# Kernel optimization log

Hardware: AMD Instinct MI355X
Metric: run time of the kernel (lower is better)

Reference implementation:

```python
import jax, jax.numpy as jnp
import numpy as np

NUM_GRIDS = 8
GRID = jnp.linspace(-2.0, 2.0, NUM_GRIDS)
DENOM = 4.0 / (NUM_GRIDS - 1)
H, D = 8, 64
Q_DIM = K_DIM = V_DIM = 512
TOT = H * D


def fastkan(x, ln_s, ln_b, sw, bw, bb):
    # LayerNorm over last dim
    mu = jnp.mean(x, axis=-1, keepdims=True)
    var = jnp.var(x, axis=-1, keepdims=True)
    xn = (x - mu) * jax.lax.rsqrt(var + 1e-5) * ln_s + ln_b
    # Gaussian RBF basis over fixed grid: [..., in, G]
    basis = jnp.exp(-jnp.square((xn[..., None] - GRID) / DENOM))
    flat = basis.reshape(*x.shape[:-1], x.shape[-1] * NUM_GRIDS)
    # spline linear + base update (silu -> linear)
    return flat @ sw.T + jax.nn.silu(x) @ bw.T + bb


def setup_inputs() -> dict:
    key = jax.random.key(0)
    keys = iter(jax.random.split(key, 32))
    B, QL, KL = 2, 2048, 2048
    inp = {
        "q": jax.random.normal(next(keys), (B, QL, Q_DIM), jnp.float32),
        "k": jax.random.normal(next(keys), (B, KL, K_DIM), jnp.float32),
        "v": jax.random.normal(next(keys), (B, KL, V_DIM), jnp.float32),
    }
    def layer(ind, outd):
        return {
            "ln_s": jnp.ones((ind,), jnp.float32),
            "ln_b": jnp.zeros((ind,), jnp.float32),
            "sw": jax.random.normal(next(keys), (outd, ind * NUM_GRIDS), jnp.float32) * (0.1 / np.sqrt(ind * NUM_GRIDS)),
            "bw": jax.random.normal(next(keys), (outd, ind), jnp.float32) / np.sqrt(ind),
            "bb": jnp.zeros((outd,), jnp.float32),
        }
    dims = {"lq": (Q_DIM, TOT), "lk": (K_DIM, TOT), "lv": (V_DIM, TOT), "lo": (TOT, Q_DIM), "lg": (Q_DIM, TOT)}
    for name, (i, o) in dims.items():
        for pn, arr in layer(i, o).items():
            inp[name + "_" + pn] = arr
    return inp


def reference(q, k, v,
              lq_ln_s, lq_ln_b, lq_sw, lq_bw, lq_bb,
              lk_ln_s, lk_ln_b, lk_sw, lk_bw, lk_bb,
              lv_ln_s, lv_ln_b, lv_sw, lv_bw, lv_bb,
              lo_ln_s, lo_ln_b, lo_sw, lo_bw, lo_bb,
              lg_ln_s, lg_ln_b, lg_sw, lg_bw, lg_bb):
    norm = D ** -0.5
    wq = fastkan(q, lq_ln_s, lq_ln_b, lq_sw, lq_bw, lq_bb).reshape(*q.shape[:-1], H, D) * norm
    wk = fastkan(k, lk_ln_s, lk_ln_b, lk_sw, lk_bw, lk_bb).reshape(*k.shape[:-1], H, D)
    # att: [b, q_len, k_len, h]; softmax over k_len (axis=-2), matching torch code
    att = jax.nn.softmax(jnp.einsum('bqhd,bkhd->bqkh', wq, wk), axis=-2)
    wv = fastkan(v, lv_ln_s, lv_ln_b, lv_sw, lv_bw, lv_bb).reshape(*v.shape[:-1], H, D)
    o = jnp.einsum('bqkh,bkhd->bqhd', att, wv).reshape(*q.shape[:-1], TOT)
    g = fastkan(q, lg_ln_s, lg_ln_b, lg_sw, lg_bw, lg_bb)
    o = jax.nn.sigmoid(g) * o
    return fastkan(o, lo_ln_s, lo_ln_b, lo_sw, lo_bw, lo_bb)
```

## Files before the change

kernel.cpp:

```cpp
#include <hip/hip_runtime.h>

typedef unsigned short u16;
typedef unsigned int u32;
typedef float f32x4 __attribute__((ext_vector_type(4)));
typedef short s16x8 __attribute__((ext_vector_type(8)));

#define IND 512
#define KSPL 4096
#define NOUT 512
#define PW 1024
#define MROWS 4096
#define LQ 2048
#define AST 72
#define NSPLIT 4

#define SWN (4096 * 512)
#define BWN (512 * 512)
#define LSTR ((size_t)(SWN + BWN + 512))

__device__ __forceinline__ float bf2f(u16 u) {
    union { u32 i; float f; } v; v.i = ((u32)u) << 16; return v.f;
}
__device__ __forceinline__ u16 f2bf(float f) {
    union { float f; u32 i; } v; v.f = f;
    u32 x = v.i;
    return (u16)((x + 0x7FFFu + ((x >> 16) & 1u)) >> 16);
}
__device__ __forceinline__ uint4 pack8(float4 a, float4 b) {
    uint4 p;
    p.x = (u32)f2bf(a.x) | ((u32)f2bf(a.y) << 16);
    p.y = (u32)f2bf(a.z) | ((u32)f2bf(a.w) << 16);
    p.z = (u32)f2bf(b.x) | ((u32)f2bf(b.y) << 16);
    p.w = (u32)f2bf(b.z) | ((u32)f2bf(b.w) << 16);
    return p;
}
__device__ __forceinline__ void gl_lds16(const u16* g, u16* l) {
    __builtin_amdgcn_global_load_lds((const __attribute__((address_space(1))) void*)g,
                                     (__attribute__((address_space(3))) void*)l, 16, 0, 0);
}

__global__ void detect_dtype(const u32* __restrict__ qraw, u32* __restrict__ flag)
{
    const int t = threadIdx.x;
    int cnt = 0;
    for (int i = t; i < 1024; i += 256) {
        u32 e = (qraw[i] >> 23) & 0xFFu;
        if (e >= 100u && e <= 140u) cnt++;
    }
    #pragma unroll
    for (int off = 32; off > 0; off >>= 1) cnt += __shfl_down(cnt, off);
    __shared__ int red[4];
    if ((t & 63) == 0) red[t >> 6] = cnt;
    __syncthreads();
    if (t == 0) flag[0] = (red[0] + red[1] + red[2] + red[3] > 512) ? 1u : 0u;
}

struct WSrc { const void* p[15]; };
__global__ __launch_bounds__(256) void convert_w(WSrc s, u16* __restrict__ wb, const u32* __restrict__ flag)
{
    const int r = blockIdx.y;
    const int l = r / 3, t = r - l * 3;
    const int n = (t == 0) ? SWN : ((t == 1) ? BWN : 512);
    const int i = (blockIdx.x * 256 + threadIdx.x) * 8;
    if (i >= n) return;
    u16* dst = wb + (size_t)l * LSTR + ((t == 0) ? 0 : ((t == 1) ? SWN : SWN + BWN)) + i;
    const void* src = s.p[r];
    if (flag[0]) {
        const float* f = (const float*)src;
        *(uint4*)dst = pack8(*(const float4*)&f[i], *(const float4*)&f[i + 4]);
    } else {
        *(uint4*)dst = *(const uint4*)&((const u16*)src)[i];
    }
}

__global__ __launch_bounds__(256) void prep_kan(
    const void* __restrict__ xvA, const void* __restrict__ lsA, const void* __restrict__ lbA,
    const void* __restrict__ xvB, const void* __restrict__ lsB, const void* __restrict__ lbB,
    u16* __restrict__ basis, u16* __restrict__ silu, const u32* __restrict__ flag)
{
    const int sel = blockIdx.x >> 12;
    const int row = blockIdx.x & 4095;
    const void* xv   = sel ? xvB : xvA;
    const void* ln_sv = sel ? lsB : lsA;
    const void* ln_bv = sel ? lbB : lbA;
    basis += (size_t)sel * MROWS * KSPL;
    silu  += (size_t)sel * MROWS * IND;
    const int t = threadIdx.x;
    const bool isf = flag[0] != 0u;
    float x0, x1;
    if (isf) {
        const float* xr = (const float*)xv + (size_t)row * IND;
        x0 = xr[t]; x1 = xr[t + 256];
    } else {
        const u16* xr = (const u16*)xv + (size_t)row * IND;
        x0 = bf2f(xr[t]); x1 = bf2f(xr[t + 256]);
    }
    float s = x0 + x1;
    float ss = x0 * x0 + x1 * x1;
    #pragma unroll
    for (int off = 32; off > 0; off >>= 1) {
        s += __shfl_down(s, off);
        ss += __shfl_down(ss, off);
    }
    __shared__ float red[8];
    const int wid = t >> 6, ln = t & 63;
    if (ln == 0) { red[wid] = s; red[4 + wid] = ss; }
    __syncthreads();
    const float tot = red[0] + red[1] + red[2] + red[3];
    const float tot2 = red[4] + red[5] + red[6] + red[7];
    const float mu = tot * (1.0f / IND);
    const float rstd = rsqrtf(tot2 * (1.0f / IND) - mu * mu + 1e-5f);
    #pragma unroll
    for (int e = 0; e < 2; e++) {
        const int i = t + e * 256;
        const float xi = (e == 0) ? x0 : x1;
        float lns, lnb;
        if (isf) {
            lns = ((const float*)ln_sv)[i];
            lnb = ((const float*)ln_bv)[i];
        } else {
            lns = bf2f(((const u16*)ln_sv)[i]);
            lnb = bf2f(((const u16*)ln_bv)[i]);
        }
        const float xn = (xi - mu) * rstd * lns + lnb;
        u16 o8[8];
        #pragma unroll
        for (int g = 0; g < 8; g++) {
            float d = (xn - (-2.0f + g * (4.0f / 7.0f))) * 1.75f;
            o8[g] = f2bf(__expf(-d * d));
        }
        uint4 pk;
        pk.x = (u32)o8[0] | ((u32)o8[1] << 16);
        pk.y = (u32)o8[2] | ((u32)o8[3] << 16);
        pk.z = (u32)o8[4] | ((u32)o8[5] << 16);
        pk.w = (u32)o8[6] | ((u32)o8[7] << 16);
        *(uint4*)(basis + (size_t)row * KSPL + i * 8) = pk;
        silu[(size_t)row * IND + i] = f2bf(xi / (1.0f + __expf(-xi)));
    }
}

__global__ __launch_bounds__(256) void prep_merge(
    const float* __restrict__ Opart, const float* __restrict__ lpart,
    const u16* __restrict__ gbuf, const void* __restrict__ ln_sv, const void* __restrict__ ln_bv,
    u16* __restrict__ basis, u16* __restrict__ silu, const u32* __restrict__ flag)
{
    const int row = blockIdx.x;
    const int b = row >> 11, qr = row & (LQ - 1);
    const int t = threadIdx.x;
    const bool isf = flag[0] != 0u;

    float xv[2];
    #pragma unroll
    for (int e = 0; e < 2; e++) {
        const int col = t + e * 256;
        const int g = b * 8 + (col >> 6);
        const int dd = col & 63;
        float o = 0.0f, l = 0.0f;
        #pragma unroll
        for (int s = 0; s < NSPLIT; s++) {
            const size_t rb = ((size_t)s * 16 + g) * LQ + qr;
            o += Opart[rb * 64 + dd];
            l += lpart[rb];
        }
        const float gv = bf2f(gbuf[(size_t)row * IND + col]);
        xv[e] = (o / l) / (1.0f + __expf(-gv));
    }
    float s = xv[0] + xv[1];
    float ss = xv[0] * xv[0] + xv[1] * xv[1];
    #pragma unroll
    for (int off = 32; off > 0; off >>= 1) {
        s += __shfl_down(s, off);
        ss += __shfl_down(ss, off);
    }
    __shared__ float red[8];
    const int wid = t >> 6, ln = t & 63;
    if (ln == 0) { red[wid] = s; red[4 + wid] = ss; }
    __syncthreads();
    const float tot = red[0] + red[1] + red[2] + red[3];
    const float tot2 = red[4] + red[5] + red[6] + red[7];
    const float mu = tot * (1.0f / IND);
    const float rstd = rsqrtf(tot2 * (1.0f / IND) - mu * mu + 1e-5f);
    #pragma unroll
    for (int e = 0; e < 2; e++) {
        const int i = t + e * 256;
        const float xi = xv[e];
        float lns, lnb;
        if (isf) {
            lns = ((const float*)ln_sv)[i];
            lnb = ((const float*)ln_bv)[i];
        } else {
            lns = bf2f(((const u16*)ln_sv)[i]);
            lnb = bf2f(((const u16*)ln_bv)[i]);
        }
        const float xn = (xi - mu) * rstd * lns + lnb;
        u16 o8[8];
        #pragma unroll
        for (int g = 0; g < 8; g++) {
            float d = (xn - (-2.0f + g * (4.0f / 7.0f))) * 1.75f;
            o8[g] = f2bf(__expf(-d * d));
        }
        uint4 pk;
        pk.x = (u32)o8[0] | ((u32)o8[1] << 16);
        pk.y = (u32)o8[2] | ((u32)o8[3] << 16);
        pk.z = (u32)o8[4] | ((u32)o8[5] << 16);
        pk.w = (u32)o8[6] | ((u32)o8[7] << 16);
        *(uint4*)(basis + (size_t)row * KSPL + i * 8) = pk;
        silu[(size_t)row * IND + i] = f2bf(xi / (1.0f + __expf(-xi)));
    }
}

struct GPair { const u16 *A1, *B1, *A2, *B2; };

template<int NZK>
__global__ __launch_bounds__(512) void gemm_big(GPair p0, GPair p1, u16* __restrict__ P)
{
    constexpr int NT1 = KSPL / (NZK * 64);
    constexpr int NT  = NT1 + IND / (NZK * 64);
    __shared__ __align__(16) u16 sA[2][256 * 64];
    __shared__ __align__(16) u16 sB[2][256 * 64];
    const int tid = threadIdx.x;
    const int lane = tid & 63;
    const int wid = tid >> 6;
    const int fm = lane & 15;
    const int quad = lane >> 4;
    const int wmbase = (wid >> 2) * 128;
    const int wnbase = (wid & 3) * 64;
    const int mbase = blockIdx.x * 256;
    const int by = blockIdx.y;
    const GPair g = (by >> 1) ? p1 : p0;
    const int nb = (by & 1) * 256;
    const int kz = blockIdx.z;
    const int k1b = kz * (KSPL / NZK);
    const int k2b = kz * (IND / NZK);

    const int srow = wid * 8 + (lane >> 3);
    const int scol = ((lane & 7) ^ (lane >> 3)) * 8;

    f32x4 acc[8][4] = {};

    {
        const u16* b0 = g.B1 + (size_t)(nb + srow) * KSPL + k1b + scol;
        const u16* a0 = g.A1 + (size_t)(mbase + srow) * KSPL + k1b + scol;
        #pragma unroll
        for (int i = 0; i < 4; i++) gl_lds16(b0 + (size_t)i * 64 * KSPL, &sB[0][i * 4096 + wid * 512]);
        #pragma unroll
        for (int i = 0; i < 4; i++) gl_lds16(a0 + (size_t)i * 64 * KSPL, &sA[0][i * 4096 + wid * 512]);
        #pragma unroll
        for (int i = 0; i < 4; i++) gl_lds16(b0 + 64 + (size_t)i * 64 * KSPL, &sB[1][i * 4096 + wid * 512]);
    }
    asm volatile("s_waitcnt vmcnt(4)" ::: "memory");
    asm volatile("s_barrier" ::: "memory");

    #pragma unroll 1
    for (int t = 0; t < NT; ++t) {
        const u16* Ac = &sA[t & 1][0];
        const u16* Bc = &sB[t & 1][0];
        u16* abuf = &sA[(t + 1) & 1][0];
        u16* bbuf = &sB[t & 1][0];

        const u16* aS = nullptr; const u16* bS = nullptr;
        size_t aStep = 0, bStep = 0;
        if (t + 1 < NT1) {
            aS = g.A1 + (size_t)(mbase + srow) * KSPL + k1b + (t + 1) * 64 + scol;
            aStep = (size_t)64 * KSPL;
        } else if (t + 1 < NT) {
            aS = g.A2 + (size_t)(mbase + srow) * IND + k2b + (t + 1 - NT1) * 64 + scol;
            aStep = (size_t)64 * IND;
        }
        if (t + 2 < NT1) {
            bS = g.B1 + (size_t)(nb + srow) * KSPL + k1b + (t + 2) * 64 + scol;
            bStep = (size_t)64 * KSPL;
        } else if (t + 2 < NT) {
            bS = g.B2 + (size_t)(nb + srow) * IND + k2b + (t + 2 - NT1) * 64 + scol;
            bStep = (size_t)64 * IND;
        }

        s16x8 bfrag[4][2];
        #pragma unroll
        for (int n = 0; n < 4; n++)
            #pragma unroll
            for (int ks = 0; ks < 2; ks++)
                bfrag[n][ks] = *(const s16x8*)&Bc[((wnbase + n * 16 + fm) << 6) +
                                                 ((((ks << 2) + quad) ^ (fm & 7)) << 3)];

        #pragma unroll
        for (int ph = 0; ph < 2; ++ph) {
            s16x8 afr[4][2];
            #pragma unroll
            for (int i = 0; i < 4; i++)
                #pragma unroll
                for (int ks = 0; ks < 2; ks++)
                    afr[i][ks] = *(const s16x8*)&Ac[((wmbase + (ph * 4 + i) * 16 + fm) << 6) +
                                                   ((((ks << 2) + quad) ^ (fm & 7)) << 3)];
            if (ph == 0) {
                if (aS) {
                    #pragma unroll
                    for (int i = 0; i < 4; i++)
                        gl_lds16(aS + (size_t)i * aStep, abuf + i * 4096 + wid * 512);
                }
            } else {
                if (bS) {
                    #pragma unroll
                    for (int i = 0; i < 4; i++)
                        gl_lds16(bS + (size_t)i * bStep, bbuf + i * 4096 + wid * 512);
                }
            }
            asm volatile("s_barrier" ::: "memory");
            __builtin_amdgcn_s_setprio(1);
            #pragma unroll
            for (int i = 0; i < 4; i++)
                #pragma unroll
                for (int n = 0; n < 4; n++) {
                    acc[ph * 4 + i][n] = __builtin_amdgcn_mfma_f32_16x16x32_bf16(afr[i][0], bfrag[n][0], acc[ph * 4 + i][n], 0, 0, 0);
                    acc[ph * 4 + i][n] = __builtin_amdgcn_mfma_f32_16x16x32_bf16(afr[i][1], bfrag[n][1], acc[ph * 4 + i][n], 0, 0, 0);
                }
            __builtin_amdgcn_s_setprio(0);
            if (ph == 1) {
                if (t < NT - 2)       asm volatile("s_waitcnt vmcnt(4)" ::: "memory");
                else if (t == NT - 2) asm volatile("s_waitcnt vmcnt(0)" ::: "memory");
            }
            asm volatile("s_barrier" ::: "memory");
        }
    }

    #pragma unroll
    for (int n = 0; n < 4; n++) {
        const int col = by * 256 + wnbase + n * 16 + fm;
        const size_t cb = ((size_t)kz * PW + col) * MROWS;
        #pragma unroll
        for (int m = 0; m < 8; m++) {
            const int row0 = mbase + wmbase + m * 16 + quad * 4;
            uint2 o;
            o.x = (u32)f2bf(acc[m][n][0]) | ((u32)f2bf(acc[m][n][1]) << 16);
            o.y = (u32)f2bf(acc[m][n][2]) | ((u32)f2bf(acc[m][n][3]) << 16);
            *(uint2*)&P[cb + row0] = o;
        }
    }
}

__global__ __launch_bounds__(256) void reduce_kan(
    const u16* __restrict__ P, const u16* __restrict__ bias0, const u16* __restrict__ bias1,
    void* __restrict__ C0, void* __restrict__ C1, float scale0, float scale1,
    int co0, int co1, int nz, const u32* __restrict__ flag, int ext_out)
{
    const int zz = blockIdx.z;
    const u16* bias = zz ? bias1 : bias0;
    void* C = zz ? C1 : C0;
    const float scale = zz ? scale1 : scale0;
    const int colofs = zz ? co1 : co0;
    __shared__ float tshf[64][65];
    const int row0 = blockIdx.x * 64;
    const int col0 = blockIdx.y * 64;
    const int tid = threadIdx.x;
    #pragma unroll
    for (int p = 0; p < 2; p++) {
        const int idx = tid + p * 256;
        const int cl = idx >> 3;
        const int r8 = (idx & 7) * 8;
        float a[8] = {};
        for (int kz = 0; kz < nz; kz++) {
            uint4 pk = *(const uint4*)&P[((size_t)kz * PW + colofs + col0 + cl) * MROWS + row0 + r8];
            const u16* pv = (const u16*)&pk;
            #pragma unroll
            for (int u = 0; u < 8; u++) a[u] += bf2f(pv[u]);
        }
        const float bi = bf2f(bias[col0 + cl]);
        #pragma unroll
        for (int u = 0; u < 8; u++) tshf[r8 + u][cl] = (a[u] + bi) * scale;
    }
    __syncthreads();
    const bool fo = ext_out && (flag[0] != 0u);
    #pragma unroll
    for (int p = 0; p < 2; p++) {
        const int idx = tid + p * 256;
        const int rl = idx >> 3;
        const int c8 = (idx & 7) * 8;
        if (fo) {
            float* Cf = (float*)C + (size_t)(row0 + rl) * NOUT + col0 + c8;
            float4 f0, f1;
            f0.x = tshf[rl][c8 + 0]; f0.y = tshf[rl][c8 + 1];
            f0.z = tshf[rl][c8 + 2]; f0.w = tshf[rl][c8 + 3];
            f1.x = tshf[rl][c8 + 4]; f1.y = tshf[rl][c8 + 5];
            f1.z = tshf[rl][c8 + 6]; f1.w = tshf[rl][c8 + 7];
            *(float4*)Cf = f0;
            *(float4*)(Cf + 4) = f1;
        } else {
            uint4 o;
            o.x = (u32)f2bf(tshf[rl][c8 + 0]) | ((u32)f2bf(tshf[rl][c8 + 1]) << 16);
            o.y = (u32)f2bf(tshf[rl][c8 + 2]) | ((u32)f2bf(tshf[rl][c8 + 3]) << 16);
            o.z = (u32)f2bf(tshf[rl][c8 + 4]) | ((u32)f2bf(tshf[rl][c8 + 5]) << 16);
            o.w = (u32)f2bf(tshf[rl][c8 + 6]) | ((u32)f2bf(tshf[rl][c8 + 7]) << 16);
            *(uint4*)&((u16*)C)[(size_t)(row0 + rl) * NOUT + col0 + c8] = o;
        }
    }
}

__global__ __launch_bounds__(256) void reduce_vt(
    const u16* __restrict__ P, const u16* __restrict__ bias, u16* __restrict__ VT,
    int colofs, int nz)
{
    const int bc = blockIdx.x;
    const int b = bc >> 9, col = bc & 511;
    const int row8 = threadIdx.x * 8;
    float a[8] = {};
    for (int kz = 0; kz < nz; kz++) {
        uint4 pk = *(const uint4*)&P[((size_t)kz * PW + colofs + col) * MROWS + b * LQ + row8];
        const u16* pv = (const u16*)&pk;
        #pragma unroll
        for (int u = 0; u < 8; u++) a[u] += bf2f(pv[u]);
    }
    const float bi = bf2f(bias[col]);
    u16 tmp[8];
    #pragma unroll
    for (int u = 0; u < 8; u++) tmp[u] = f2bf(a[u] + bi);
    *(uint4*)&VT[(size_t)bc * LQ + row8] = *(const uint4*)tmp;
}

__global__ __launch_bounds__(256) void attn4(
    const u16* __restrict__ wqp, const u16* __restrict__ wkp, const u16* __restrict__ VT,
    float* __restrict__ Opart, float* __restrict__ lpart)
{
    __shared__ __align__(16) u16 Ks[64 * 64];
    __shared__ __align__(16) u16 Vs[64 * 64];
    __shared__ __align__(16) u16 Ps[4][32 * AST];

    const int tid = threadIdx.x;
    const int lane = tid & 63;
    const int wid = tid >> 6;
    const int quad = lane >> 4;
    const int fm = lane & 15;
    const int srow8 = lane >> 3;
    const int schk = (lane & 7) ^ (lane >> 3);
    const int qb = blockIdx.x * 128;
    const int g = blockIdx.y;
    const int s = blockIdx.z;
    const int b = g >> 3, h = g & 7;
    const size_t qkbase = ((size_t)b * LQ) * 512 + h * 64;
    const size_t vtbase = (size_t)g * 64 * LQ;
    const int kvlen = LQ / NSPLIT, kv0 = s * kvlen;

    s16x8 aq[2][2];
    #pragma unroll
    for (int qi = 0; qi < 2; qi++)
        #pragma unroll
        for (int ks = 0; ks < 2; ks++)
            aq[qi][ks] = *(const s16x8*)&wqp[qkbase +
                (size_t)(qb + wid * 32 + qi * 16 + fm) * 512 + ks * 32 + quad * 8];
    s16x8 ones;
    #pragma unroll
    for (int i = 0; i < 8; i++) ones[i] = (short)0x3F80;

    f32x4 oacc[2][4] = {};
    f32x4 lacc[2] = {};

    for (int kt = 0; kt < kvlen / 64; kt++) {
        const int kb = kv0 + kt * 64;
        #pragma unroll
        for (int gg = 0; gg < 2; gg++) {
            const int r = wid * 16 + gg * 8 + srow8;
            gl_lds16(&wkp[qkbase + (size_t)(kb + r) * 512 + schk * 8], &Ks[(wid * 16 + gg * 8) * 64]);
            gl_lds16(&VT[vtbase + (size_t)r * LQ + kb + schk * 8],     &Vs[(wid * 16 + gg * 8) * 64]);
        }
        __syncthreads();

        #pragma unroll
        for (int j = 0; j < 4; j++) {
            f32x4 z0 = {}, z1 = {};
            #pragma unroll
            for (int ks = 0; ks < 2; ks++) {
                s16x8 bk = *(const s16x8*)&Ks[((j * 16 + fm) << 6) +
                                              ((((ks << 2) + quad) ^ (fm & 7)) << 3)];
                z0 = __builtin_amdgcn_mfma_f32_16x16x32_bf16(aq[0][ks], bk, z0, 0, 0, 0);
                z1 = __builtin_amdgcn_mfma_f32_16x16x32_bf16(aq[1][ks], bk, z1, 0, 0, 0);
            }
            #pragma unroll
            for (int r = 0; r < 4; r++) {
                union { float f; u32 i; } u0, u1;
                u0.f = __expf(z0[r] - 12.0f);
                u1.f = __expf(z1[r] - 12.0f);
                Ps[wid][(quad * 4 + r) * AST + j * 16 + fm]        = (u16)(u0.i >> 16);
                Ps[wid][(16 + quad * 4 + r) * AST + j * 16 + fm]   = (u16)(u1.i >> 16);
            }
        }

        s16x8 ap[2][2];
        #pragma unroll
        for (int qi = 0; qi < 2; qi++)
            #pragma unroll
            for (int ks = 0; ks < 2; ks++)
                ap[qi][ks] = *(const s16x8*)&Ps[wid][(qi * 16 + fm) * AST + ks * 32 + quad * 8];
        #pragma unroll
        for (int jd = 0; jd < 4; jd++)
            #pragma unroll
            for (int ks = 0; ks < 2; ks++) {
                s16x8 bv = *(const s16x8*)&Vs[((jd * 16 + fm) << 6) +
                                              ((((ks << 2) + quad) ^ (fm & 7)) << 3)];
                oacc[0][jd] = __builtin_amdgcn_mfma_f32_16x16x32_bf16(ap[0][ks], bv, oacc[0][jd], 0, 0, 0);
                oacc[1][jd] = __builtin_amdgcn_mfma_f32_16x16x32_bf16(ap[1][ks], bv, oacc[1][jd], 0, 0, 0);
            }
        #pragma unroll
        for (int qi = 0; qi < 2; qi++)
            #pragma unroll
            for (int ks = 0; ks < 2; ks++)
                lacc[qi] = __builtin_amdgcn_mfma_f32_16x16x32_bf16(ap[qi][ks], ones, lacc[qi], 0, 0, 0);
        __syncthreads();
    }

    const size_t obase = ((size_t)s * 16 + g) * LQ;
    #pragma unroll
    for (int qi = 0; qi < 2; qi++) {
        #pragma unroll
        for (int jd = 0; jd < 4; jd++)
            #pragma unroll
            for (int r = 0; r < 4; r++) {
                const int qrow = qb + wid * 32 + qi * 16 + quad * 4 + r;
                Opart[(obase + qrow) * 64 + jd * 16 + fm] = oacc[qi][jd][r];
            }
        if (fm == 0) {
            #pragma unroll
            for (int r = 0; r < 4; r++) {
                const int qrow = qb + wid * 32 + qi * 16 + quad * 4 + r;
                lpart[obase + qrow] = lacc[qi][r];
            }
        }
    }
}

extern "C" void kernel_launch(void* const* d_in, const int* in_sizes, int n_in,
                              void* d_out, int out_size, void* d_ws, size_t ws_size,
                              hipStream_t stream)
{
    const void* q = d_in[0];
    const void* k = d_in[1];
    const void* v = d_in[2];
    auto P = [&](int i) { return (const void*)d_in[i]; };

    const size_t WB_BYTES  = 5 * LSTR * 2;
    const size_t BAS_BYTES = (size_t)MROWS * KSPL * 2 * 2;
    const size_t SIL_BYTES = (size_t)MROWS * IND * 2 * 2;
    const size_t PART_B    = (size_t)8 * MROWS * PW * 2;
    const size_t VT_B      = (size_t)16 * 64 * LQ * 2;
    const size_t OPART_B   = (size_t)NSPLIT * 16 * LQ * 64 * 4;

    char* base = (char*)d_ws;
    u32*  flag  = (u32*)base;
    u16*  wb    = (u16*)(base + 4096);
    u16*  basis = (u16*)((char*)wb + WB_BYTES);
    u16*  silu  = (u16*)((char*)basis + BAS_BYTES);
    u16*  wq    = (u16*)((char*)silu + SIL_BYTES);
    u16*  wk    = wq + (size_t)MROWS * NOUT;
    u16*  gbuf  = wk + (size_t)MROWS * NOUT;
    u16*  part  = gbuf + (size_t)MROWS * NOUT;
    u16*  VT    = (u16*)((char*)part + PART_B);
    float* Opart = (float*)((char*)VT + VT_B);
    float* lpart = (float*)((char*)Opart + OPART_B);

    u16* basisB = basis + (size_t)MROWS * KSPL;
    u16* siluB  = silu + (size_t)MROWS * IND;

    detect_dtype<<<1, 256, 0, stream>>>((const u32*)q, flag);

    WSrc srcs;
    const int lbase[5] = {3, 8, 13, 18, 23};
    for (int l = 0; l < 5; l++) {
        srcs.p[l * 3 + 0] = d_in[lbase[l] + 2];
        srcs.p[l * 3 + 1] = d_in[lbase[l] + 3];
        srcs.p[l * 3 + 2] = d_in[lbase[l] + 4];
    }
    convert_w<<<dim3(SWN / 2048, 15), 256, 0, stream>>>(srcs, wb, flag);

    auto swb = [&](int l) { return wb + (size_t)l * LSTR; };
    auto bwb = [&](int l) { return wb + (size_t)l * LSTR + SWN; };
    auto bbb = [&](int l) { return wb + (size_t)l * LSTR + SWN + BWN; };
    dim3 gg4(MROWS / 256, 4, 4);
    dim3 gg8(MROWS / 256, 2, 8);
    dim3 rg(MROWS / 64, NOUT / 64);
    dim3 rg2(MROWS / 64, NOUT / 64, 2);

    prep_kan<<<MROWS, 256, 0, stream>>>(q, P(3), P(4), nullptr, nullptr, nullptr, basis, silu, flag);
    {
        GPair pq{basis, swb(0), silu, bwb(0)};
        GPair pg{basis, swb(4), silu, bwb(4)};
        (gemm_big<4>)<<<gg4, 512, 0, stream>>>(pq, pg, part);
    }
    reduce_kan<<<rg2, 256, 0, stream>>>(part, bbb(0), bbb(4), wq, gbuf, 0.125f, 1.0f, 0, 512, 4, flag, 0);

    prep_kan<<<2 * MROWS, 256, 0, stream>>>(k, P(8), P(9), v, P(13), P(14), basis, silu, flag);
    {
        GPair pk{basis, swb(1), silu, bwb(1)};
        GPair pv{basisB, swb(2), siluB, bwb(2)};
        (gemm_big<4>)<<<gg4, 512, 0, stream>>>(pk, pv, part);
    }
    reduce_kan<<<rg, 256, 0, stream>>>(part, bbb(1), bbb(1), wk, wk, 1.0f, 1.0f, 0, 0, 4, flag, 0);
    reduce_vt<<<1024, 256, 0, stream>>>(part, bbb(2), VT, 512, 4);

    attn4<<<dim3(LQ / 128, 16, NSPLIT), 256, 0, stream>>>(wq, wk, VT, Opart, lpart);

    prep_merge<<<MROWS, 256, 0, stream>>>(Opart, lpart, gbuf, P(18), P(19), basis, silu, flag);
    {
        GPair po{basis, swb(3), silu, bwb(3)};
        (gemm_big<8>)<<<gg8, 512, 0, stream>>>(po, po, part);
    }
    reduce_kan<<<rg, 256, 0, stream>>>(part, bbb(3), bbb(3), d_out, d_out, 1.0f, 1.0f, 0, 0, 8, flag, 1);
}
```

Baseline: 378.7 us.

## Merge Q/G/K/V KAN prep and GEMMs into single launches with fewer K-splits

The q, k and v LayerNorm/RBF basis preparation now runs in one prep_kan launch writing three basis/silu sets. The four projection GEMMs (q, gate, k, v) run in one gemm_big launch indexed through a GQuad parameter, with the split-K factor lowered from 4 to 2 and the partial-buffer width made a runtime parameter. This removes two launches and the serialization between the q and k/v phases, and halves the partial-sum traffic the reductions must read. In exchange each block does a longer K loop and the workspace grows to hold a third basis set.

```diff
diff --git a/kernel.cpp b/kernel.cpp
--- a/kernel.cpp
+++ b/kernel.cpp
@@ -8,7 +8,6 @@
 #define IND 512
 #define KSPL 4096
 #define NOUT 512
-#define PW 1024
 #define MROWS 4096
 #define LQ 2048
 #define AST 72
@@ -76,13 +75,14 @@
 __global__ __launch_bounds__(256) void prep_kan(
     const void* __restrict__ xvA, const void* __restrict__ lsA, const void* __restrict__ lbA,
     const void* __restrict__ xvB, const void* __restrict__ lsB, const void* __restrict__ lbB,
+    const void* __restrict__ xvC, const void* __restrict__ lsC, const void* __restrict__ lbC,
     u16* __restrict__ basis, u16* __restrict__ silu, const u32* __restrict__ flag)
 {
     const int sel = blockIdx.x >> 12;
     const int row = blockIdx.x & 4095;
-    const void* xv   = sel ? xvB : xvA;
-    const void* ln_sv = sel ? lsB : lsA;
-    const void* ln_bv = sel ? lbB : lbA;
+    const void* xv    = (sel == 0) ? xvA : ((sel == 1) ? xvB : xvC);
+    const void* ln_sv = (sel == 0) ? lsA : ((sel == 1) ? lsB : lsC);
+    const void* ln_bv = (sel == 0) ? lbA : ((sel == 1) ? lbB : lbC);
     basis += (size_t)sel * MROWS * KSPL;
     silu  += (size_t)sel * MROWS * IND;
     const int t = threadIdx.x;
@@ -210,9 +210,10 @@
 }
 
 struct GPair { const u16 *A1, *B1, *A2, *B2; };
+struct GQuad { GPair p[4]; };
 
 template<int NZK>
-__global__ __launch_bounds__(512) void gemm_big(GPair p0, GPair p1, u16* __restrict__ P)
+__global__ __launch_bounds__(512) void gemm_big(GQuad qs, u16* __restrict__ P, int pw)
 {
     constexpr int NT1 = KSPL / (NZK * 64);
     constexpr int NT  = NT1 + IND / (NZK * 64);
@@ -227,7 +228,7 @@
     const int wnbase = (wid & 3) * 64;
     const int mbase = blockIdx.x * 256;
     const int by = blockIdx.y;
-    const GPair g = (by >> 1) ? p1 : p0;
+    const GPair g = qs.p[by >> 1];
     const int nb = (by & 1) * 256;
     const int kz = blockIdx.z;
     const int k1b = kz * (KSPL / NZK);
@@ -326,7 +327,7 @@
     #pragma unroll
     for (int n = 0; n < 4; n++) {
         const int col = by * 256 + wnbase + n * 16 + fm;
-        const size_t cb = ((size_t)kz * PW + col) * MROWS;
+        const size_t cb = ((size_t)kz * pw + col) * MROWS;
         #pragma unroll
         for (int m = 0; m < 8; m++) {
             const int row0 = mbase + wmbase + m * 16 + quad * 4;
@@ -341,7 +342,7 @@
 __global__ __launch_bounds__(256) void reduce_kan(
     const u16* __restrict__ P, const u16* __restrict__ bias0, const u16* __restrict__ bias1,
     void* __restrict__ C0, void* __restrict__ C1, float scale0, float scale1,
-    int co0, int co1, int nz, const u32* __restrict__ flag, int ext_out)
+    int co0, int co1, int nz, int pw, const u32* __restrict__ flag, int ext_out)
 {
     const int zz = blockIdx.z;
     const u16* bias = zz ? bias1 : bias0;
@@ -359,7 +360,7 @@
         const int r8 = (idx & 7) * 8;
         float a[8] = {};
         for (int kz = 0; kz < nz; kz++) {
-            uint4 pk = *(const uint4*)&P[((size_t)kz * PW + colofs + col0 + cl) * MROWS + row0 + r8];
+            uint4 pk = *(const uint4*)&P[((size_t)kz * pw + colofs + col0 + cl) * MROWS + row0 + r8];
             const u16* pv = (const u16*)&pk;
             #pragma unroll
             for (int u = 0; u < 8; u++) a[u] += bf2f(pv[u]);
@@ -397,14 +398,14 @@
 
 __global__ __launch_bounds__(256) void reduce_vt(
     const u16* __restrict__ P, const u16* __restrict__ bias, u16* __restrict__ VT,
-    int colofs, int nz)
+    int colofs, int nz, int pw)
 {
     const int bc = blockIdx.x;
     const int b = bc >> 9, col = bc & 511;
     const int row8 = threadIdx.x * 8;
     float a[8] = {};
     for (int kz = 0; kz < nz; kz++) {
-        uint4 pk = *(const uint4*)&P[((size_t)kz * PW + colofs + col) * MROWS + b * LQ + row8];
+        uint4 pk = *(const uint4*)&P[((size_t)kz * pw + colofs + col) * MROWS + b * LQ + row8];
         const u16* pv = (const u16*)&pk;
         #pragma unroll
         for (int u = 0; u < 8; u++) a[u] += bf2f(pv[u]);
@@ -536,9 +537,9 @@
     auto P = [&](int i) { return (const void*)d_in[i]; };
 
     const size_t WB_BYTES  = 5 * LSTR * 2;
-    const size_t BAS_BYTES = (size_t)MROWS * KSPL * 2 * 2;
-    const size_t SIL_BYTES = (size_t)MROWS * IND * 2 * 2;
-    const size_t PART_B    = (size_t)8 * MROWS * PW * 2;
+    const size_t BAS_SET   = (size_t)MROWS * KSPL * 2;
+    const size_t SIL_SET   = (size_t)MROWS * IND * 2;
+    const size_t PART_B    = (size_t)2 * MROWS * 2048 * 2;
     const size_t VT_B      = (size_t)16 * 64 * LQ * 2;
     const size_t OPART_B   = (size_t)NSPLIT * 16 * LQ * 64 * 4;
 
@@ -546,8 +547,8 @@
     u32*  flag  = (u32*)base;
     u16*  wb    = (u16*)(base + 4096);
     u16*  basis = (u16*)((char*)wb + WB_BYTES);
-    u16*  silu  = (u16*)((char*)basis + BAS_BYTES);
-    u16*  wq    = (u16*)((char*)silu + SIL_BYTES);
+    u16*  silu  = (u16*)((char*)basis + 3 * BAS_SET);
+    u16*  wq    = (u16*)((char*)silu + 3 * SIL_SET);
     u16*  wk    = wq + (size_t)MROWS * NOUT;
     u16*  gbuf  = wk + (size_t)MROWS * NOUT;
     u16*  part  = gbuf + (size_t)MROWS * NOUT;
@@ -556,7 +557,9 @@
     float* lpart = (float*)((char*)Opart + OPART_B);
 
     u16* basisB = basis + (size_t)MROWS * KSPL;
+    u16* basisC = basisB + (size_t)MROWS * KSPL;
     u16* siluB  = silu + (size_t)MROWS * IND;
+    u16* siluC  = siluB + (size_t)MROWS * IND;
 
     detect_dtype<<<1, 256, 0, stream>>>((const u32*)q, flag);
 
@@ -572,34 +575,36 @@
     auto swb = [&](int l) { return wb + (size_t)l * LSTR; };
     auto bwb = [&](int l) { return wb + (size_t)l * LSTR + SWN; };
     auto bbb = [&](int l) { return wb + (size_t)l * LSTR + SWN + BWN; };
-    dim3 gg4(MROWS / 256, 4, 4);
-    dim3 gg8(MROWS / 256, 2, 8);
+    dim3 ggM(MROWS / 256, 8, 2);
+    dim3 ggL(MROWS / 256, 2, 8);
     dim3 rg(MROWS / 64, NOUT / 64);
     dim3 rg2(MROWS / 64, NOUT / 64, 2);
 
-    prep_kan<<<MROWS, 256, 0, stream>>>(q, P(3), P(4), nullptr, nullptr, nullptr, basis, silu, flag);
+    prep_kan<<<3 * MROWS, 256, 0, stream>>>(q, P(3), P(4), k, P(8), P(9), v, P(13), P(14),
+                                            basis, silu, flag);
     {
-        GPair pq{basis, swb(0), silu, bwb(0)};
-        GPair pg{basis, swb(4), silu, bwb(4)};
-        (gemm_big<4>)<<<gg4, 512, 0, stream>>>(pq, pg, part);
-    }
-    reduce_kan<<<rg2, 256, 0, stream>>>(part, bbb(0), bbb(4), wq, gbuf, 0.125f, 1.0f, 0, 512, 4, flag, 0);
-
-    prep_kan<<<2 * MROWS, 256, 0, stream>>>(k, P(8), P(9), v, P(13), P(14), basis, silu, flag);
-    {
-        GPair pk{basis, swb(1), silu, bwb(1)};
-        GPair pv{basisB, swb(2), siluB, bwb(2)};
-        (gemm_big<4>)<<<gg4, 512, 0, stream>>>(pk, pv, part);
-    }
-    reduce_kan<<<rg, 256, 0, stream>>>(part, bbb(1), bbb(1), wk, wk, 1.0f, 1.0f, 0, 0, 4, flag, 0);
-    reduce_vt<<<1024, 256, 0, stream>>>(part, bbb(2), VT, 512, 4);
+        GQuad m;
+        m.p[0] = {basis,  swb(0), silu,  bwb(0)};
+        m.p[1] = {basis,  swb(4), silu,  bwb(4)};
+        m.p[2] = {basisB, swb(1), siluB, bwb(1)};
+        m.p[3] = {basisC, swb(2), siluC, bwb(2)};
+        (gemm_big<2>)<<<ggM, 512, 0, stream>>>(m, part, 2048);
+    }
+    reduce_kan<<<rg2, 256, 0, stream>>>(part, bbb(0), bbb(4), wq, gbuf, 0.125f, 1.0f,
+                                        0, 512, 2, 2048, flag, 0);
+    reduce_kan<<<rg, 256, 0, stream>>>(part, bbb(1), bbb(1), wk, wk, 1.0f, 1.0f,
+                                       1024, 1024, 2, 2048, flag, 0);
+    reduce_vt<<<1024, 256, 0, stream>>>(part, bbb(2), VT, 1536, 2, 2048);
 
     attn4<<<dim3(LQ / 128, 16, NSPLIT), 256, 0, stream>>>(wq, wk, VT, Opart, lpart);
 
     prep_merge<<<MROWS, 256, 0, stream>>>(Opart, lpart, gbuf, P(18), P(19), basis, silu, flag);
     {
-        GPair po{basis, swb(3), silu, bwb(3)};
-        (gemm_big<8>)<<<gg8, 512, 0, stream>>>(po, po, part);
-    }
-    reduce_kan<<<rg, 256, 0, stream>>>(part, bbb(3), bbb(3), d_out, d_out, 1.0f, 1.0f, 0, 0, 8, flag, 1);
-}
+        GQuad o;
+        o.p[0] = {basis, swb(3), silu, bwb(3)};
+        o.p[1] = o.p[0]; o.p[2] = o.p[0]; o.p[3] = o.p[0];
+        (gemm_big<8>)<<<ggL, 512, 0, stream>>>(o, part, 512);
+    }
+    reduce_kan<<<rg, 256, 0, stream>>>(part, bbb(3), bbb(3), d_out, d_out, 1.0f, 1.0f,
+                                       0, 0, 8, 512, flag, 1);
+}
```

Result: faster. 352.7 us (-6.9%).
